# Performance work log

Measured on AMD Instinct MI355X. Metric: run time of the kernel, lower is better.

Reference implementation:

```python
import jax, jax.numpy as jnp
import numpy as np

EMBED_DIM = 1024
NUM_HEADS = 16
PROJ_DIM = EMBED_DIM // NUM_HEADS


def setup_inputs() -> dict:
    key = jax.random.key(0)
    ks = jax.random.split(key, 11)
    B, S, D = 2, 2048, EMBED_DIM
    scale = 1.0 / np.sqrt(D)
    inp = {
        'q': jax.random.normal(ks[0], (B, S, D), jnp.float32),
        'k': jax.random.normal(ks[1], (B, S, D), jnp.float32),
        'v': jax.random.normal(ks[2], (B, S, D), jnp.float32),
        'Wq': jax.random.normal(ks[3], (D, D), jnp.float32) * scale,
        'bq': jnp.zeros((D,), jnp.float32),
        'Wk': jax.random.normal(ks[4], (D, D), jnp.float32) * scale,
        'bk': jnp.zeros((D,), jnp.float32),
        'Wv': jax.random.normal(ks[5], (D, D), jnp.float32) * scale,
        'bv': jnp.zeros((D,), jnp.float32),
        'Wo': jax.random.normal(ks[6], (D, D), jnp.float32) * scale,
        'bo': jnp.zeros((D,), jnp.float32),
        'use_causal_mask': 1,
    }
    return inp


def _split_heads(x, B):
    # [B, S, D] -> [B, H, S, Pd]
    return x.reshape(B, -1, NUM_HEADS, PROJ_DIM).transpose(0, 2, 1, 3)


def reference(q, k, v, Wq, bq, Wk, bk, Wv, bv, Wo, bo, use_causal_mask):
    B, S, D = q.shape
    qh = _split_heads(q @ Wq + bq, B)
    kh = _split_heads(k @ Wk + bk, B)
    vh = _split_heads(v @ Wv + bv, B)
    # scaled dot-product attention; scores [B, H, S, S]
    logits = jnp.einsum('bhqd,bhkd->bhqk', qh, kh) / jnp.sqrt(
        jnp.asarray(PROJ_DIM, jnp.float32))
    if use_causal_mask:
        # faithful to source: logits += log(tril * 1e-9 + 1e-9)
        tril = jnp.tril(jnp.ones((S, S), dtype=logits.dtype))
        logits = logits + jnp.log(tril * 1e-9 + 1e-9)
    attn = jax.nn.softmax(logits, axis=-1)
    out = jnp.einsum('bhqk,bhkd->bhqd', attn, vh)
    out = out.transpose(0, 2, 1, 3).reshape(B, S, D)
    return out @ Wo + bo
```

## Files before the change

kernel.cpp:

```cpp
#include <hip/hip_runtime.h>
#include <hip/hip_bf16.h>
#include <stdint.h>

#define EMBED 1024
#define NH    16
#define PD    64
#define BATCH 2
#define SEQ   2048

typedef unsigned short u16;
typedef __attribute__((ext_vector_type(8))) short bf16x8;
typedef __attribute__((ext_vector_type(4))) float f32x4;

#define WAITALL() __builtin_amdgcn_s_waitcnt(0)

__device__ __forceinline__ float b2f(u16 x) {
  unsigned u = ((unsigned)x) << 16;
  return __builtin_bit_cast(float, u);
}
__device__ __forceinline__ u16 cvtb(float x) {
  __bf16 h = (__bf16)x;
  return __builtin_bit_cast(u16, h);
}
__device__ __forceinline__ float loadIn(const void* p, size_t i, int isf32) {
  return isf32 ? ((const float*)p)[i] : b2f(((const u16*)p)[i]);
}
__device__ __forceinline__ void async16(const void* g, void* l) {
  __builtin_amdgcn_global_load_lds((const __attribute__((address_space(1))) void*)g,
                                   (__attribute__((address_space(3))) void*)l,
                                   16, 0, 0);
}
__device__ __forceinline__ int detect_f32(const void* q) {
  unsigned w0 = ((const unsigned*)q)[threadIdx.x & 63];
  unsigned e = (w0 >> 7) & 0xffu;
  unsigned long long m = __ballot(e >= 110 && e <= 135);
  return (__popcll(m) < 32) ? 1 : 0;
}

__global__ __launch_bounds__(256) void conv_fused(
    const void* q, const void* k, const void* v,
    const void* Wq, const void* Wk, const void* Wv, const void* Wo,
    u16* qb, u16* kb, u16* vb, u16* WT_all) {
  __shared__ float sh[64][65];
  const int isf32 = detect_f32(q);

  if (blockIdx.y < 3) {
    size_t i = ((size_t)blockIdx.x * 256 + threadIdx.x) * 8;
    const void* src = (blockIdx.y == 0) ? q : (blockIdx.y == 1) ? k : v;
    u16* dst = (blockIdx.y == 0) ? qb : (blockIdx.y == 1) ? kb : vb;
    u16 tmp[8];
    if (isf32) {
      const float* s = (const float*)src + i;
      float4 a = *(const float4*)s;
      float4 b = *(const float4*)(s + 4);
      tmp[0] = cvtb(a.x); tmp[1] = cvtb(a.y); tmp[2] = cvtb(a.z); tmp[3] = cvtb(a.w);
      tmp[4] = cvtb(b.x); tmp[5] = cvtb(b.y); tmp[6] = cvtb(b.z); tmp[7] = cvtb(b.w);
    } else {
      const uint4 r = *(const uint4*)((const u16*)src + i);
      *(uint4*)tmp = r;
    }
    *(uint4*)(dst + i) = *(uint4*)tmp;
    return;
  }

  if (blockIdx.x >= 1024) return;
  const int z = blockIdx.x >> 8;
  const int xy = blockIdx.x & 255;
  const int bx = xy & 15, by = xy >> 4;
  const void* W = (z == 0) ? Wq : (z == 1) ? Wk : (z == 2) ? Wv : Wo;
  u16* WT = WT_all + (size_t)z * EMBED * EMBED;
  int r0 = by * 64, c0 = bx * 64;
  int col = threadIdx.x & 63;
  int rb  = threadIdx.x >> 6;
#pragma unroll
  for (int i = 0; i < 16; i++) {
    int row = i * 4 + rb;
    sh[row][col] = loadIn(W, (size_t)(r0 + row) * EMBED + c0 + col, isf32);
  }
  __syncthreads();
#pragma unroll
  for (int i = 0; i < 16; i++) {
    int row = i * 4 + rb;
    WT[(size_t)(c0 + row) * EMBED + r0 + col] = cvtb(sh[col][row]);
  }
}

__device__ __forceinline__ void gemm_stage(const u16* __restrict__ A,
                                           const u16* __restrict__ Bt,
                                           int tm, int tn, int kt,
                                           u16* As, u16* Bs, int tid) {
#pragma unroll
  for (int i = 0; i < 4; i++) {
    int c = i * 256 + tid;
    int row = c >> 3;
    int col = ((c & 7) << 3) ^ ((row & 7) << 3);
    async16(A + (size_t)(tm + row) * EMBED + kt + col, As + c * 8);
    async16(Bt + (size_t)(tn + row) * EMBED + kt + col, Bs + c * 8);
  }
}

__device__ __forceinline__ void gemm_compute(const u16* As, const u16* Bs,
                                             int wm, int wn, int l15, int quad,
                                             int rbx, f32x4 acc[4][4]) {
#pragma unroll
  for (int ks = 0; ks < 64; ks += 32) {
    int ko = (ks + quad * 8) ^ rbx;
    bf16x8 af[4], bf[4];
#pragma unroll
    for (int mt = 0; mt < 4; mt++)
      af[mt] = *(const bf16x8*)(As + (wm + mt * 16 + l15) * 64 + ko);
#pragma unroll
    for (int nt = 0; nt < 4; nt++)
      bf[nt] = *(const bf16x8*)(Bs + (wn + nt * 16 + l15) * 64 + ko);
#pragma unroll
    for (int mt = 0; mt < 4; mt++)
#pragma unroll
      for (int nt = 0; nt < 4; nt++)
        acc[mt][nt] = __builtin_amdgcn_mfma_f32_16x16x32_bf16(
            af[mt], bf[nt], acc[mt][nt], 0, 0, 0);
  }
}

__global__ __launch_bounds__(512, 2) void qkv_gemm(
    const u16* qb, const u16* kb, const u16* vb, const u16* wts,
    const void* bq, const void* bk, const void* bv,
    u16* Qh, u16* Kh, u16* Vt, const void* qorig) {
  __shared__ __align__(16) u16 lds[3 * 16384];
  const int isf32 = detect_f32(qorig);

  const int lid = blockIdx.x;
  const int mhi = lid & 7;
  const int mlo = (lid >> 3) & 1;
  const int vx = (lid >> 4) & 3;
  const int z = lid >> 6;
  const int vm = mhi * 2 + mlo;
  const int tm = vm * 256, tn = vx * 256;

  const u16* A = (z == 0) ? qb : (z == 1) ? kb : vb;
  const u16* Bt = wts + (size_t)z * EMBED * EMBED;
  const void* bias = (z == 0) ? bq : (z == 1) ? bk : bv;

  const int tid = threadIdx.x, lane = tid & 63, wv = tid >> 6;
  const int wm = (wv >> 2) * 128, wn = (wv & 3) * 64;
  const int l15 = lane & 15, quad = lane >> 4;
  const int rbx32 = (lane & 3) << 3;

  f32x4 acc[8][4];
  f32x4 zz = {0.f, 0.f, 0.f, 0.f};
#pragma unroll
  for (int i = 0; i < 8; i++)
#pragma unroll
    for (int j = 0; j < 4; j++) acc[i][j] = zz;

#define QKV_STAGE(t_, bb_)                                                    \
  {                                                                           \
    const int kt_ = (t_) * 32;                                                \
    u16* Ab_ = lds + (bb_) * 16384;                                           \
    u16* Bb_ = Ab_ + 8192;                                                    \
    _Pragma("unroll") for (int i = 0; i < 2; i++) {                           \
      int c = i * 512 + tid;                                                  \
      int row = c >> 2;                                                       \
      int col = (((c & 3) ^ (row & 3)) << 3);                                 \
      async16(A + (size_t)(tm + row) * EMBED + kt_ + col, Ab_ + c * 8);       \
      async16(Bt + (size_t)(tn + row) * EMBED + kt_ + col, Bb_ + c * 8);      \
    }                                                                         \
  }

  QKV_STAGE(0, 0);
  QKV_STAGE(1, 1);

  int b0 = 0, b1 = 1, b2 = 2;

  for (int t = 0; t < 32; t++) {
    if (t == 31) {
      asm volatile("s_waitcnt vmcnt(0)" ::: "memory");
    } else {
      asm volatile("s_waitcnt vmcnt(4)" ::: "memory");
    }
    __builtin_amdgcn_sched_barrier(0);
    __builtin_amdgcn_s_barrier();

    if (t + 2 < 32) QKV_STAGE(t + 2, b2);

    const u16* Asc = lds + b0 * 16384;
    const u16* Bsc = Asc + 8192;
    bf16x8 af[8], bf[4];
#pragma unroll
    for (int mt = 0; mt < 8; mt++) {
      int row = wm + mt * 16 + l15;
      af[mt] = *(const bf16x8*)(Asc + row * 32 + ((quad * 8) ^ rbx32));
    }
#pragma unroll
    for (int nt = 0; nt < 4; nt++) {
      int row = wn + nt * 16 + l15;
      bf[nt] = *(const bf16x8*)(Bsc + row * 32 + ((quad * 8) ^ rbx32));
    }
#pragma unroll
    for (int mt = 0; mt < 8; mt++)
#pragma unroll
      for (int nt = 0; nt < 4; nt++)
        acc[mt][nt] = __builtin_amdgcn_mfma_f32_16x16x32_bf16(
            af[mt], bf[nt], acc[mt][nt], 0, 0, 0);

    int tmp = b0; b0 = b1; b1 = b2; b2 = tmp;
  }
#undef QKV_STAGE

  int rbase = tm + wm + (quad << 2);
  int cbase = tn + wn + l15;
  if (z < 2) {
    u16* dst = (z == 0) ? Qh : Kh;
#pragma unroll
    for (int mt = 0; mt < 8; mt++)
#pragma unroll
      for (int nt = 0; nt < 4; nt++) {
        int col = cbase + nt * 16;
        float bv_ = loadIn(bias, col, isf32);
        int h = col >> 6, p = col & 63;
#pragma unroll
        for (int j = 0; j < 4; j++) {
          int row = rbase + mt * 16 + j;
          int b = row >> 11, s = row & 2047;
          dst[(((size_t)(b * NH + h) * SEQ) + s) * PD + p] =
              cvtb(acc[mt][nt][j] + bv_);
        }
      }
  } else {
#pragma unroll
    for (int mt = 0; mt < 8; mt++)
#pragma unroll
      for (int nt = 0; nt < 4; nt++) {
        int col = cbase + nt * 16;
        float bv_ = loadIn(bias, col, isf32);
        int h = col >> 6, p = col & 63;
        int row0 = rbase + mt * 16;
        int b = row0 >> 11, s0 = row0 & 2047;
        int beta = s0 >> 5, w = s0 & 31;
        int pos = (beta << 5) + (((w >> 2) & 3) << 3) + ((w >> 4) << 2);
        ushort4 pk;
        pk.x = cvtb(acc[mt][nt][0] + bv_);
        pk.y = cvtb(acc[mt][nt][1] + bv_);
        pk.z = cvtb(acc[mt][nt][2] + bv_);
        pk.w = cvtb(acc[mt][nt][3] + bv_);
        *(ushort4*)(Vt + ((size_t)(b * NH + h) * PD + p) * SEQ + pos) = pk;
      }
  }
}

__global__ __launch_bounds__(256, 4) void attn(const u16* __restrict__ Qh,
                                               const u16* __restrict__ Kh,
                                               const u16* __restrict__ Vt,
                                               u16* __restrict__ O,
                                               const int* __restrict__ maskflag) {
  __shared__ __align__(16) u16 sh[5 * 64 * 64];
  u16* const Vbase = sh + 3 * 4096;
  u16* const Qs    = sh + 2 * 4096;

  const int lid = blockIdx.x + (blockIdx.y << 5);
  const int xcd = lid & 7, j = lid >> 3;
  const int bh = (xcd << 2) | (j & 3);
  const int qt = (j >> 2) * 64;

  const int tid = threadIdx.x, lane = tid & 63, wv = tid >> 6;
  const int qh = wv & 1;
  const int kh = wv >> 1;
  const int l15 = lane & 15, quad = lane >> 4;
  const int rbx = (lane & 7) << 3;
  const size_t head = (size_t)bh * SEQ * PD;
  const bool causal = (maskflag[0] != 0);
  const float C = 0.18033688011112042f;

  const int c0 = tid, c1 = 256 + tid;
  const int r0 = c0 >> 3, r1 = c1 >> 3;
  const int x0 = ((c0 & 7) << 3) ^ ((r0 & 7) << 3);
  const int x1 = ((c1 & 7) << 3) ^ ((r1 & 7) << 3);

  async16(Qh + head + (size_t)(qt + r0) * PD + x0, Qs + c0 * 8);
  async16(Qh + head + (size_t)(qt + r1) * PD + x1, Qs + c1 * 8);
  async16(Kh + head + (size_t)r0 * PD + x0, sh + c0 * 8);
  async16(Kh + head + (size_t)r1 * PD + x1, sh + c1 * 8);
  async16(Vt + head + (size_t)r0 * SEQ + x0, Vbase + c0 * 8);
  async16(Vt + head + (size_t)r1 * SEQ + x1, Vbase + c1 * 8);
  async16(Kh + head + (size_t)(64 + r0) * PD + x0, sh + 4096 + c0 * 8);
  async16(Kh + head + (size_t)(64 + r1) * PD + x1, sh + 4096 + c1 * 8);
  __syncthreads();

  bf16x8 qf[2][2];
#pragma unroll
  for (int ks = 0; ks < 2; ks++) {
    int ko = (ks * 32 + quad * 8) ^ rbx;
    qf[ks][0] = *(const bf16x8*)(Qs + (qh * 32 + l15) * 64 + ko);
    qf[ks][1] = *(const bf16x8*)(Qs + (qh * 32 + 16 + l15) * 64 + ko);
  }
  __syncthreads();

  float lacc[2] = {0.f, 0.f};
  f32x4 oacc[4][2];
  f32x4 z4 = {0.f, 0.f, 0.f, 0.f};
#pragma unroll
  for (int mt = 0; mt < 4; mt++)
#pragma unroll
    for (int qx = 0; qx < 2; qx++) oacc[mt][qx] = z4;

  const int qrow0 = qt + qh * 32 + l15;

  int b0 = 0, b1 = 1, b2 = 2;

  for (int t = 0; t < SEQ / 64; t++) {
    if (t == SEQ / 64 - 1) {
      asm volatile("s_waitcnt vmcnt(0)" ::: "memory");
    } else {
      asm volatile("s_waitcnt vmcnt(2)" ::: "memory");
    }
    __builtin_amdgcn_sched_barrier(0);
    __builtin_amdgcn_s_barrier();

    const int k0 = t * 64;
    if (t + 1 < SEQ / 64) {
      const int kn = k0 + 64;
      u16* Vn = Vbase + ((t + 1) & 1) * 4096;
      async16(Vt + head + (size_t)r0 * SEQ + kn + x0, Vn + c0 * 8);
      async16(Vt + head + (size_t)r1 * SEQ + kn + x1, Vn + c1 * 8);
    }
    if (t + 2 < SEQ / 64) {
      const int kn = k0 + 128;
      u16* Kn = sh + b2 * 4096;
      async16(Kh + head + (size_t)(kn + r0) * PD + x0, Kn + c0 * 8);
      async16(Kh + head + (size_t)(kn + r1) * PD + x1, Kn + c1 * 8);
    }
    const u16* Ksc = sh + b0 * 4096;
    const u16* Vsc = Vbase + (t & 1) * 4096;

    f32x4 st[2][2];
#pragma unroll
    for (int kx = 0; kx < 2; kx++)
#pragma unroll
      for (int qx = 0; qx < 2; qx++) st[kx][qx] = z4;
    __builtin_amdgcn_s_setprio(1);
#pragma unroll
    for (int ks = 0; ks < 2; ks++) {
      int ko = (ks * 32 + quad * 8) ^ rbx;
#pragma unroll
      for (int kx = 0; kx < 2; kx++) {
        bf16x8 kf = *(const bf16x8*)(Ksc + (kh * 32 + kx * 16 + l15) * 64 + ko);
        st[kx][0] = __builtin_amdgcn_mfma_f32_16x16x32_bf16(kf, qf[ks][0], st[kx][0], 0, 0, 0);
        st[kx][1] = __builtin_amdgcn_mfma_f32_16x16x32_bf16(kf, qf[ks][1], st[kx][1], 0, 0, 0);
      }
    }
    __builtin_amdgcn_s_setprio(0);

    const int mode = !causal ? 0 : (k0 > qt + 63 ? 2 : (k0 + 63 <= qt ? 0 : 1));
    const float ub = (mode == 2) ? -17.f : -16.f;
    unsigned pw[2][4];
#pragma unroll
    for (int kx = 0; kx < 2; kx++) {
#pragma unroll
      for (int qx = 0; qx < 2; qx++) {
        const int qrow = qrow0 + qx * 16;
        float p[4];
#pragma unroll
        for (int r = 0; r < 4; r++) {
          float bias = ub;
          if (mode == 1) {
            int kappa = k0 + kh * 32 + kx * 16 + 4 * quad + r;
            bias = (kappa > qrow) ? -17.f : -16.f;
          }
          p[r] = exp2f(fmaf(st[kx][qx][r], C, bias));
        }
        lacc[qx] += (p[0] + p[1]) + (p[2] + p[3]);
        pw[qx][kx * 2 + 0] =
            (unsigned)cvtb(p[0]) | ((unsigned)cvtb(p[1]) << 16);
        pw[qx][kx * 2 + 1] =
            (unsigned)cvtb(p[2]) | ((unsigned)cvtb(p[3]) << 16);
      }
    }

    __builtin_amdgcn_s_setprio(1);
    bf16x8 pf0 = __builtin_bit_cast(bf16x8,
        (uint4){pw[0][0], pw[0][1], pw[0][2], pw[0][3]});
    bf16x8 pf1 = __builtin_bit_cast(bf16x8,
        (uint4){pw[1][0], pw[1][1], pw[1][2], pw[1][3]});
#pragma unroll
    for (int mt = 0; mt < 4; mt++) {
      int row = mt * 16 + l15;
      int chunk = ((kh << 2) + quad) ^ (row & 7);
      bf16x8 vf = *(const bf16x8*)(Vsc + row * 64 + (chunk << 3));
      oacc[mt][0] = __builtin_amdgcn_mfma_f32_16x16x32_bf16(vf, pf0, oacc[mt][0], 0, 0, 0);
      oacc[mt][1] = __builtin_amdgcn_mfma_f32_16x16x32_bf16(vf, pf1, oacc[mt][1], 0, 0, 0);
    }
    __builtin_amdgcn_s_setprio(0);

    int tmp = b0; b0 = b1; b1 = b2; b2 = tmp;
  }

  __syncthreads();

#pragma unroll
  for (int qx = 0; qx < 2; qx++) {
    lacc[qx] += __shfl_xor(lacc[qx], 16, 64);
    lacc[qx] += __shfl_xor(lacc[qx], 32, 64);
  }

  float* red = (float*)sh;
  if (kh == 1) {
#pragma unroll
    for (int mt = 0; mt < 4; mt++)
#pragma unroll
      for (int qx = 0; qx < 2; qx++)
        *(f32x4*)(red + qh * 2048 + (mt * 2 + qx) * 256 + lane * 4) =
            oacc[mt][qx];
    red[4096 + qh * 128 + lane] = lacc[0];
    red[4096 + qh * 128 + 64 + lane] = lacc[1];
  }
  __syncthreads();
  if (kh == 0) {
    float l0 = lacc[0] + red[4096 + qh * 128 + lane];
    float l1 = lacc[1] + red[4096 + qh * 128 + 64 + lane];
    float inv[2] = {1.f / l0, 1.f / l1};
    const int b = bh >> 4, h = bh & 15;
#pragma unroll
    for (int mt = 0; mt < 4; mt++) {
#pragma unroll
      for (int qx = 0; qx < 2; qx++) {
        f32x4 o = oacc[mt][qx] +
                  *(const f32x4*)(red + qh * 2048 + (mt * 2 + qx) * 256 + lane * 4);
        int qrow = qrow0 + qx * 16;
        ushort4 w;
        w.x = cvtb(o[0] * inv[qx]);
        w.y = cvtb(o[1] * inv[qx]);
        w.z = cvtb(o[2] * inv[qx]);
        w.w = cvtb(o[3] * inv[qx]);
        *(ushort4*)(O + ((size_t)b * SEQ + qrow) * EMBED + h * PD + mt * 16 +
                    4 * quad) = w;
      }
    }
  }
}

__global__ __launch_bounds__(256) void out_gemm(const u16* __restrict__ Ob,
                                                const u16* __restrict__ WoT,
                                                const void* __restrict__ bo,
                                                void* __restrict__ out,
                                                const void* __restrict__ qorig) {
  __shared__ __align__(16) u16 lds[4 * 128 * 64];
  const int isf32 = detect_f32(qorig);

  const int lid = blockIdx.x + (blockIdx.y << 3);
  const int mgrp = lid & 7;
  const int vx = (lid >> 3) & 7;
  const int vm = lid >> 6;
  int tm = (mgrp * 4 + vm) * 128, tn = vx * 128;

  const int tid = threadIdx.x, lane = tid & 63, wv = tid >> 6;
  const int wm = (wv >> 1) * 64, wn = (wv & 1) * 64;
  const int l15 = lane & 15, quad = lane >> 4;
  const int rbx = (lane & 7) << 3;
  f32x4 acc[4][4];
  f32x4 zz = {0.f, 0.f, 0.f, 0.f};
#pragma unroll
  for (int i = 0; i < 4; i++)
#pragma unroll
    for (int j = 0; j < 4; j++) acc[i][j] = zz;

  gemm_stage(Ob, WoT, tm, tn, 0, lds, lds + 8192, tid);
  WAITALL();
  __syncthreads();
  for (int kt = 0; kt < EMBED; kt += 64) {
    const int cur = (kt >> 6) & 1;
    u16* curb = lds + cur * 16384;
    if (kt + 64 < EMBED)
      gemm_stage(Ob, WoT, tm, tn, kt + 64, lds + (cur ^ 1) * 16384,
                 lds + (cur ^ 1) * 16384 + 8192, tid);
    gemm_compute(curb, curb + 8192, wm, wn, l15, quad, rbx, acc);
    WAITALL();
    __syncthreads();
  }

  int rbase = tm + wm + (quad << 2);
  int cbase = tn + wn + l15;
#pragma unroll
  for (int mt = 0; mt < 4; mt++)
#pragma unroll
    for (int nt = 0; nt < 4; nt++) {
      int col = cbase + nt * 16;
      float bv_ = loadIn(bo, col, isf32);
#pragma unroll
      for (int j = 0; j < 4; j++) {
        int row = rbase + mt * 16 + j;
        float val = acc[mt][nt][j] + bv_;
        size_t off = (size_t)row * EMBED + col;
        if (isf32) ((float*)out)[off] = val;
        else       ((u16*)out)[off]   = cvtb(val);
      }
    }
}

extern "C" void kernel_launch(void* const* d_in, const int* in_sizes, int n_in,
                              void* d_out, int out_size, void* d_ws, size_t ws_size,
                              hipStream_t stream) {
  const void* q  = d_in[0];
  const void* k  = d_in[1];
  const void* v  = d_in[2];
  const void* Wq = d_in[3];
  const void* bq = d_in[4];
  const void* Wk = d_in[5];
  const void* bk = d_in[6];
  const void* Wv = d_in[7];
  const void* bv = d_in[8];
  const void* Wo = d_in[9];
  const void* bo = d_in[10];
  const int* msk = (const int*)d_in[11];

  char* ws = (char*)d_ws;
  u16*  qb    = (u16*)(ws + 64);
  u16*  kb    = qb + (size_t)4194304;
  u16*  vb    = kb + (size_t)4194304;
  u16*  WT    = vb + (size_t)4194304;
  u16*  Qh    = WT + (size_t)4194304;
  u16*  Kh    = Qh + (size_t)4194304;
  u16*  Vt    = Kh + (size_t)4194304;
  u16*  Ob    = Vt + (size_t)4194304;

  conv_fused<<<dim3(2048, 4), 256, 0, stream>>>(q, k, v, Wq, Wk, Wv, Wo,
                                                qb, kb, vb, WT);
  qkv_gemm<<<dim3(192), 512, 0, stream>>>(qb, kb, vb, WT, bq, bk, bv,
                                          Qh, Kh, Vt, q);
  attn<<<dim3(32, 32), 256, 0, stream>>>(Qh, Kh, Vt, Ob, msk);
  out_gemm<<<dim3(8, 32), 256, 0, stream>>>(Ob, WT + (size_t)3 * 1048576,
                                            bo, d_out, q);
}
```

Measured before the change: 254.9 us.

## Triple-buffer out_gemm with 32-wide K tiles and partial vmcnt waits

Replaces the double-buffered 64-wide K loop in the output projection GEMM with a three-stage ring of 32-wide K tiles. Each iteration waits only for the oldest in-flight stage via s_waitcnt vmcnt(4) and uses a single barrier, so global loads overlap more with MFMA work. LDS usage drops from four to three 8K-element buffers, which may raise occupancy. The cost is twice as many loop iterations and barriers, a new swizzle for 32-wide rows, and a correctness dependence on the exact count of async loads per stage.

Result: no change. 255.1 us (+0.1%).

```diff
diff --git a/kernel.cpp b/kernel.cpp
--- a/kernel.cpp
+++ b/kernel.cpp
@@ -82,42 +82,6 @@
   for (int i = 0; i < 16; i++) {
     int row = i * 4 + rb;
     WT[(size_t)(c0 + row) * EMBED + r0 + col] = cvtb(sh[col][row]);
-  }
-}
-
-__device__ __forceinline__ void gemm_stage(const u16* __restrict__ A,
-                                           const u16* __restrict__ Bt,
-                                           int tm, int tn, int kt,
-                                           u16* As, u16* Bs, int tid) {
-#pragma unroll
-  for (int i = 0; i < 4; i++) {
-    int c = i * 256 + tid;
-    int row = c >> 3;
-    int col = ((c & 7) << 3) ^ ((row & 7) << 3);
-    async16(A + (size_t)(tm + row) * EMBED + kt + col, As + c * 8);
-    async16(Bt + (size_t)(tn + row) * EMBED + kt + col, Bs + c * 8);
-  }
-}
-
-__device__ __forceinline__ void gemm_compute(const u16* As, const u16* Bs,
-                                             int wm, int wn, int l15, int quad,
-                                             int rbx, f32x4 acc[4][4]) {
-#pragma unroll
-  for (int ks = 0; ks < 64; ks += 32) {
-    int ko = (ks + quad * 8) ^ rbx;
-    bf16x8 af[4], bf[4];
-#pragma unroll
-    for (int mt = 0; mt < 4; mt++)
-      af[mt] = *(const bf16x8*)(As + (wm + mt * 16 + l15) * 64 + ko);
-#pragma unroll
-    for (int nt = 0; nt < 4; nt++)
-      bf[nt] = *(const bf16x8*)(Bs + (wn + nt * 16 + l15) * 64 + ko);
-#pragma unroll
-    for (int mt = 0; mt < 4; mt++)
-#pragma unroll
-      for (int nt = 0; nt < 4; nt++)
-        acc[mt][nt] = __builtin_amdgcn_mfma_f32_16x16x32_bf16(
-            af[mt], bf[nt], acc[mt][nt], 0, 0, 0);
   }
 }
 
@@ -442,7 +406,7 @@
                                                 const void* __restrict__ bo,
                                                 void* __restrict__ out,
                                                 const void* __restrict__ qorig) {
-  __shared__ __align__(16) u16 lds[4 * 128 * 64];
+  __shared__ __align__(16) u16 lds[3 * 8192];
   const int isf32 = detect_f32(qorig);
 
   const int lid = blockIdx.x + (blockIdx.y << 3);
@@ -454,7 +418,7 @@
   const int tid = threadIdx.x, lane = tid & 63, wv = tid >> 6;
   const int wm = (wv >> 1) * 64, wn = (wv & 1) * 64;
   const int l15 = lane & 15, quad = lane >> 4;
-  const int rbx = (lane & 7) << 3;
+  const int rbx32 = (lane & 3) << 3;
   f32x4 acc[4][4];
   f32x4 zz = {0.f, 0.f, 0.f, 0.f};
 #pragma unroll
@@ -462,19 +426,59 @@
 #pragma unroll
     for (int j = 0; j < 4; j++) acc[i][j] = zz;
 
-  gemm_stage(Ob, WoT, tm, tn, 0, lds, lds + 8192, tid);
-  WAITALL();
-  __syncthreads();
-  for (int kt = 0; kt < EMBED; kt += 64) {
-    const int cur = (kt >> 6) & 1;
-    u16* curb = lds + cur * 16384;
-    if (kt + 64 < EMBED)
-      gemm_stage(Ob, WoT, tm, tn, kt + 64, lds + (cur ^ 1) * 16384,
-                 lds + (cur ^ 1) * 16384 + 8192, tid);
-    gemm_compute(curb, curb + 8192, wm, wn, l15, quad, rbx, acc);
-    WAITALL();
-    __syncthreads();
-  }
+#define OUT_STAGE(t_, bb_)                                                    \
+  {                                                                           \
+    const int kt_ = (t_) * 32;                                                \
+    u16* Ab_ = lds + (bb_) * 8192;                                            \
+    u16* Bb_ = Ab_ + 4096;                                                    \
+    _Pragma("unroll") for (int i = 0; i < 2; i++) {                           \
+      int c = i * 256 + tid;                                                  \
+      int row = c >> 2;                                                       \
+      int col = (((c & 3) ^ (row & 3)) << 3);                                 \
+      async16(Ob + (size_t)(tm + row) * EMBED + kt_ + col, Ab_ + c * 8);      \
+      async16(WoT + (size_t)(tn + row) * EMBED + kt_ + col, Bb_ + c * 8);     \
+    }                                                                         \
+  }
+
+  OUT_STAGE(0, 0);
+  OUT_STAGE(1, 1);
+
+  int b0 = 0, b1 = 1, b2 = 2;
+
+  for (int t = 0; t < 32; t++) {
+    if (t == 31) {
+      asm volatile("s_waitcnt vmcnt(0)" ::: "memory");
+    } else {
+      asm volatile("s_waitcnt vmcnt(4)" ::: "memory");
+    }
+    __builtin_amdgcn_sched_barrier(0);
+    __builtin_amdgcn_s_barrier();
+
+    if (t + 2 < 32) OUT_STAGE(t + 2, b2);
+
+    const u16* Asc = lds + b0 * 8192;
+    const u16* Bsc = Asc + 4096;
+    bf16x8 af[4], bf[4];
+#pragma unroll
+    for (int mt = 0; mt < 4; mt++) {
+      int row = wm + mt * 16 + l15;
+      af[mt] = *(const bf16x8*)(Asc + row * 32 + ((quad * 8) ^ rbx32));
+    }
+#pragma unroll
+    for (int nt = 0; nt < 4; nt++) {
+      int row = wn + nt * 16 + l15;
+      bf[nt] = *(const bf16x8*)(Bsc + row * 32 + ((quad * 8) ^ rbx32));
+    }
+#pragma unroll
+    for (int mt = 0; mt < 4; mt++)
+#pragma unroll
+      for (int nt = 0; nt < 4; nt++)
+        acc[mt][nt] = __builtin_amdgcn_mfma_f32_16x16x32_bf16(
+            af[mt], bf[nt], acc[mt][nt], 0, 0, 0);
+
+    int tmp = b0; b0 = b1; b1 = b2; b2 = tmp;
+  }
+#undef OUT_STAGE
 
   int rbase = tm + wm + (quad << 2);
   int cbase = tn + wn + l15;
```
